# Kernel optimization log

Hardware: AMD Instinct MI355X
Metric: run time of the kernel (lower is better)

The kernel has to match this reference:

```python
import jax, jax.numpy as jnp
import numpy as np

_EPS = 1e-10
_SHIFT = 1  # init kwarg `shift`

R, N = 65536, 192  # rays, samples per ray


def setup_inputs() -> dict:
    key = jax.random.key(0)
    k1, k2, k3 = jax.random.split(key, 3)
    rgbs = jax.random.uniform(k1, (R, N, 3), dtype=jnp.float32)
    densities = jax.random.uniform(k2, (R, N), dtype=jnp.float32)
    points_3d = jax.random.normal(k3, (R, N, 3), dtype=jnp.float32)
    return {"rgbs": rgbs, "densities": densities, "points_3d": points_3d}


def reference(rgbs, densities, points_3d):
    num_ray_points = points_3d.shape[-2]
    pts = points_3d.reshape(-1, num_ray_points, 3)
    # regular sampling: single scalar step size taken from the first ray
    delta = jnp.linalg.norm(pts[0, 1, :] - pts[0, 0, :])
    alpha = 1.0 - jnp.exp(-densities * delta)          # (R, N)
    trans = jnp.cumprod(1.0 - alpha + _EPS, axis=-1)   # transmittance, (R, N)
    trans = jnp.roll(trans, _SHIFT, axis=-1)
    trans = trans.at[..., :_SHIFT].set(1.0)
    weights = trans * alpha                            # (R, N)
    rgbs_rendered = jnp.sum(weights[..., None] * rgbs, axis=-2)  # (R, 3)
    return rgbs_rendered
```

## Files before the change

kernel.cpp:

```cpp
#include <hip/hip_runtime.h>
#include <math.h>


constexpr int N_SAMP = 192;
constexpr float EPS = 1e-10f;

__global__ __launch_bounds__(256) void render_kernel(
    const float* __restrict__ rgbs,
    const float* __restrict__ dens,
    const float* __restrict__ pts,
    float* __restrict__ out,
    int R)
{
    const int lane = threadIdx.x & 63;
    const int ray  = (blockIdx.x * blockDim.x + threadIdx.x) >> 6;
    if (ray >= R) return;

    const float dx = pts[3] - pts[0];
    const float dy = pts[4] - pts[1];
    const float dz = pts[5] - pts[2];
    const float delta = sqrtf(dx * dx + dy * dy + dz * dz);

    const float* __restrict__ d_ray   = dens + (size_t)ray * N_SAMP;
    const float* __restrict__ rgb_ray = rgbs + (size_t)ray * N_SAMP * 3;

    float a[3], t[3];
#pragma unroll
    for (int j = 0; j < 3; ++j) {
        const float d  = d_ray[j * 64 + lane];
        const float al = 1.0f - __expf(-d * delta);
        a[j] = al;
        t[j] = 1.0f - al + EPS;
    }

    float sr = 0.0f, sg = 0.0f, sb = 0.0f;
    float carry = 1.0f;
#pragma unroll
    for (int j = 0; j < 3; ++j) {
        float incl = t[j];
#pragma unroll
        for (int off = 1; off < 64; off <<= 1) {
            const float up = __shfl_up(incl, off, 64);
            incl *= (lane >= off) ? up : 1.0f;
        }
        float excl = __shfl_up(incl, 1, 64);
        if (lane == 0) excl = 1.0f;

        const float w = carry * excl * a[j];

        const float* __restrict__ p = rgb_ray + (size_t)(j * 64 + lane) * 3;
        sr += w * p[0];
        sg += w * p[1];
        sb += w * p[2];

        carry *= __shfl(incl, 63, 64);
    }

#pragma unroll
    for (int off = 32; off >= 1; off >>= 1) {
        sr += __shfl_down(sr, off, 64);
        sg += __shfl_down(sg, off, 64);
        sb += __shfl_down(sb, off, 64);
    }
    if (lane == 0) {
        float* o = out + (size_t)ray * 3;
        o[0] = sr;
        o[1] = sg;
        o[2] = sb;
    }
}

extern "C" void kernel_launch(void* const* d_in, const int* in_sizes, int n_in,
                              void* d_out, int out_size, void* d_ws, size_t ws_size,
                              hipStream_t stream) {
    const float* rgbs = (const float*)d_in[0];
    const float* dens = (const float*)d_in[1];
    const float* pts  = (const float*)d_in[2];
    float* out = (float*)d_out;

    const int R = in_sizes[1] / N_SAMP;

    const int waves_per_block = 4;
    dim3 block(256);
    dim3 grid((R + waves_per_block - 1) / waves_per_block);
    render_kernel<<<grid, block, 0, stream>>>(rgbs, dens, pts, out, R);
}
```

Before: 34.68 us.

## Give each lane three contiguous samples and use one wave scan

Each lane now owns three consecutive samples rather than three strided ones. It computes their local transmittance product serially and runs a single 64-lane multiplicative scan, where before it ran three scans linked by carries. The rgb and density loads become contiguous per-lane chunks of 3 and 9 floats, which the compiler may be able to vectorize. Coalescing per instruction changes: each lane now reads with a stride of 12 or 36 bytes, though the wave as a whole still covers a contiguous region. The rounding order of the product also changes slightly.

```diff
diff --git a/kernel.cpp b/kernel.cpp
--- a/kernel.cpp
+++ b/kernel.cpp
@@ -21,40 +21,41 @@
     const float dz = pts[5] - pts[2];
     const float delta = sqrtf(dx * dx + dy * dy + dz * dz);
 
-    const float* __restrict__ d_ray   = dens + (size_t)ray * N_SAMP;
-    const float* __restrict__ rgb_ray = rgbs + (size_t)ray * N_SAMP * 3;
+    const float* __restrict__ dp = dens + (size_t)ray * N_SAMP + 3 * lane;
+    const float* __restrict__ rp = rgbs + ((size_t)ray * N_SAMP + 3 * lane) * 3;
+
+    float dv[3];
+#pragma unroll
+    for (int i = 0; i < 3; ++i) dv[i] = dp[i];
+
+    float r[9];
+#pragma unroll
+    for (int i = 0; i < 9; ++i) r[i] = rp[i];
 
     float a[3], t[3];
 #pragma unroll
-    for (int j = 0; j < 3; ++j) {
-        const float d  = d_ray[j * 64 + lane];
-        const float al = 1.0f - __expf(-d * delta);
-        a[j] = al;
-        t[j] = 1.0f - al + EPS;
+    for (int i = 0; i < 3; ++i) {
+        a[i] = 1.0f - __expf(-dv[i] * delta);
+        t[i] = 1.0f - a[i] + EPS;
     }
 
-    float sr = 0.0f, sg = 0.0f, sb = 0.0f;
-    float carry = 1.0f;
+    float incl = t[0] * t[1] * t[2];
 #pragma unroll
-    for (int j = 0; j < 3; ++j) {
-        float incl = t[j];
-#pragma unroll
-        for (int off = 1; off < 64; off <<= 1) {
-            const float up = __shfl_up(incl, off, 64);
-            incl *= (lane >= off) ? up : 1.0f;
-        }
-        float excl = __shfl_up(incl, 1, 64);
-        if (lane == 0) excl = 1.0f;
+    for (int off = 1; off < 64; off <<= 1) {
+        const float up = __shfl_up(incl, off, 64);
+        incl *= (lane >= off) ? up : 1.0f;
+    }
+    float excl = __shfl_up(incl, 1, 64);
+    if (lane == 0) excl = 1.0f;
 
-        const float w = carry * excl * a[j];
+    const float w0 = excl * a[0];
+    const float e1 = excl * t[0];
+    const float w1 = e1 * a[1];
+    const float w2 = e1 * t[1] * a[2];
 
-        const float* __restrict__ p = rgb_ray + (size_t)(j * 64 + lane) * 3;
-        sr += w * p[0];
-        sg += w * p[1];
-        sb += w * p[2];
-
-        carry *= __shfl(incl, 63, 64);
-    }
+    float sr = w0 * r[0] + w1 * r[3] + w2 * r[6];
+    float sg = w0 * r[1] + w1 * r[4] + w2 * r[7];
+    float sb = w0 * r[2] + w1 * r[5] + w2 * r[8];
 
 #pragma unroll
     for (int off = 32; off >= 1; off >>= 1) {
```

Measured after the change: 34.25 us. No clear change (-1.2%).
